# Optimization experiments

Measured on AMD Instinct MI355X. Metric: run time of the kernel, lower is better.

## Reference

```python
import jax, jax.numpy as jnp
import numpy as np
import math

N, E, H, A = 50000, 800000, 128, 8
D = H // A


def setup_inputs() -> dict:
    key = jax.random.key(0)
    ks = jax.random.split(key, 12)
    q = jax.random.normal(ks[0], (N, H), dtype=jnp.float32)
    k = jax.random.normal(ks[1], (N, H), dtype=jnp.float32)
    v = jax.random.normal(ks[2], (N, H), dtype=jnp.float32)
    Wq = jax.random.normal(ks[3], (H, H), dtype=jnp.float32) * 0.05
    bq = jax.random.normal(ks[4], (H,), dtype=jnp.float32) * 0.05
    Wk = jax.random.normal(ks[5], (H, H), dtype=jnp.float32) * 0.05
    bk = jax.random.normal(ks[6], (H,), dtype=jnp.float32) * 0.05
    Wv = jax.random.normal(ks[7], (H, H), dtype=jnp.float32) * 0.05
    bv = jax.random.normal(ks[8], (H,), dtype=jnp.float32) * 0.05
    # Ensure every node id appears at least once in q_indices so that
    # q_indices.unique() == arange(N) and the output shape is static [N, H].
    tail = jax.random.randint(ks[9], (E - N,), 0, N)
    q_indices = jnp.concatenate([jnp.arange(N), tail]).astype(jnp.int32)
    k_indices = jax.random.randint(ks[10], (E,), 0, N).astype(jnp.int32)
    return {"q": q, "k": k, "v": v, "Wq": Wq, "bq": bq, "Wk": Wk, "bk": bk,
            "Wv": Wv, "bv": bv, "q_indices": q_indices, "k_indices": k_indices}


def reference(q, k, v, Wq, bq, Wk, bk, Wv, bv, q_indices, k_indices):
    n = q.shape[0]
    # Gather node features per edge (irregular access).
    qe = q[q_indices]            # [E, H]
    ke = k[k_indices]            # [E, H]
    ve = v[k_indices]            # [E, H]
    # Linear projections (torch Linear: x @ W.T + b), split heads -> [E, A, D].
    Q = (qe @ Wq.T + bq).reshape(-1, A, D)
    K = (ke @ Wk.T + bk).reshape(-1, A, D)
    V = (ve @ Wv.T + bv).reshape(-1, A, D)
    # Per-edge scaled dot-product scores: [E, A].
    scores = jnp.einsum('ead,ead->ea', Q, K) / math.sqrt(D)
    # Segment softmax over edges sharing the same destination node
    # (faithful to the original: plain exp, no max subtraction).
    ex = jnp.exp(scores)                                        # [E, A]
    denom = jax.ops.segment_sum(ex, q_indices, num_segments=n)  # [N, A]
    probs = ex / denom[q_indices]                               # [E, A]
    # Scatter-aggregate weighted values per destination node: [N, A, D].
    ctx = jax.ops.segment_sum(probs[:, :, None] * V, q_indices, num_segments=n)
    # Merge heads -> [N, H].
    return ctx.reshape(n, A * D)
```

## Files before the change

### kernel.cpp

```cpp
#include <hip/hip_runtime.h>
#include <hip/hip_bf16.h>

#define HDIM 128
#define LDS_STRIDE 136

typedef __attribute__((ext_vector_type(8))) short bf16x8;
typedef __attribute__((ext_vector_type(4))) float f32x4;

__device__ inline unsigned short f2bf(float f) {
    return __builtin_bit_cast(unsigned short, __float2bfloat16(f));
}
__device__ inline float bflo(unsigned u) { return __uint_as_float(u << 16); }
__device__ inline float bfhi(unsigned u) { return __uint_as_float(u & 0xffff0000u); }

__global__ void init_kernel(int* __restrict__ deg, int n,
                            const float* __restrict__ Wq, const float* __restrict__ Wk,
                            const float* __restrict__ Wv, unsigned short* __restrict__ Wopt) {
    int i = blockIdx.x * 256 + threadIdx.x;
    if (i < n) deg[i] = 0;
    if (i < 3 * HDIM * HDIM) {
        int j  = i & 7;
        int l  = (i >> 3) & 63;
        int ks = (i >> 9) & 3;
        int nt = (i >> 11) & 7;
        int m  = i >> 14;
        const float* W = (m == 0) ? Wq : (m == 1) ? Wk : Wv;
        int row = nt * 16 + (l & 15);
        int col = ks * 32 + ((l >> 4) << 3) + j;
        Wopt[i] = f2bf(W[row * HDIM + col]);
    }
}

__global__ void proj_deg(const float* __restrict__ qin, const float* __restrict__ kin,
                         const float* __restrict__ vin, const unsigned short* __restrict__ Wopt,
                         const float* __restrict__ bq, const float* __restrict__ bk,
                         const float* __restrict__ bv,
                         unsigned short* __restrict__ Qb, unsigned short* __restrict__ Kb,
                         unsigned short* __restrict__ Vb,
                         const int* __restrict__ qidx, int* __restrict__ deg,
                         int* __restrict__ rank, int E, int n, int nbx)
{
    __shared__ unsigned short tile[64 * LDS_STRIDE];

    if (blockIdx.y == 3) {
        int e = blockIdx.x * 256 + threadIdx.x;
        if (e < E) rank[e] = atomicAdd(&deg[qidx[e]], 1);
        return;
    }
    if (blockIdx.x >= (unsigned)nbx) return;

    const int tid  = threadIdx.x;
    const int lane = tid & 63;
    const int wv   = tid >> 6;
    const int m    = blockIdx.y;
    const long node0 = (long)blockIdx.x * 64;

    const float* x = (m == 0) ? qin : (m == 1) ? kin : vin;
    const float* b = (m == 0) ? bq  : (m == 1) ? bk  : bv;
    unsigned short* O = (m == 0) ? Qb : (m == 1) ? Kb : Vb;
    const unsigned short* Wm = Wopt + (size_t)m * HDIM * HDIM;

    #pragma unroll
    for (int it = 0; it < 8; ++it) {
        int f   = it * 256 + tid;
        int row = f >> 5;
        int c4  = f & 31;
        long node = node0 + row;
        float4 val = make_float4(0.f, 0.f, 0.f, 0.f);
        if (node < n) val = ((const float4*)(x + node * HDIM))[c4];
        ushort4 h;
        h.x = f2bf(val.x); h.y = f2bf(val.y); h.z = f2bf(val.z); h.w = f2bf(val.w);
        *(ushort4*)&tile[row * LDS_STRIDE + c4 * 4] = h;
    }
    __syncthreads();

    const int r15  = lane & 15;
    const int quad = lane >> 4;

    bf16x8 af[4];
    #pragma unroll
    for (int ks = 0; ks < 4; ++ks)
        af[ks] = *(const bf16x8*)&tile[(wv * 16 + r15) * LDS_STRIDE + quad * 8 + ks * 32];

    f32x4 acc[8];
    #pragma unroll
    for (int nt = 0; nt < 8; ++nt) {
        acc[nt] = (f32x4){0.f, 0.f, 0.f, 0.f};
        #pragma unroll
        for (int ks = 0; ks < 4; ++ks) {
            const bf16x8 wfrag =
                *(const bf16x8*)(Wm + ((size_t)((nt * 4 + ks) * 64) + lane) * 8);
            acc[nt] = __builtin_amdgcn_mfma_f32_16x16x32_bf16(af[ks], wfrag, acc[nt], 0, 0, 0);
        }
    }
    __syncthreads();

    #pragma unroll
    for (int nt = 0; nt < 8; ++nt) {
        const int c = nt * 16 + r15;
        const float bias = b[c];
        #pragma unroll
        for (int r = 0; r < 4; ++r)
            tile[(wv * 16 + quad * 4 + r) * LDS_STRIDE + c] = f2bf(acc[nt][r] + bias);
    }
    __syncthreads();

    #pragma unroll
    for (int it = 0; it < 4; ++it) {
        int g   = it * 256 + tid;
        int row = g >> 4;
        int col = (g & 15) * 8;
        long node = node0 + row;
        if (node < n) {
            ushort4 lo = *(const ushort4*)&tile[row * LDS_STRIDE + col];
            ushort4 hi = *(const ushort4*)&tile[row * LDS_STRIDE + col + 4];
            uint4 out4;
            out4.x = (unsigned)lo.x | ((unsigned)lo.y << 16);
            out4.y = (unsigned)lo.z | ((unsigned)lo.w << 16);
            out4.z = (unsigned)hi.x | ((unsigned)hi.y << 16);
            out4.w = (unsigned)hi.z | ((unsigned)hi.w << 16);
            *(uint4*)&O[node * HDIM + col] = out4;
        }
    }
}

__global__ void scan_block(const int* __restrict__ deg, int* __restrict__ offs,
                           int* __restrict__ bsum, int n) {
    __shared__ int ws[17];
    const int tid = threadIdx.x;
    const int lane = tid & 63, wv = tid >> 6;
    int i = blockIdx.x * 1024 + tid;
    int v = (i < n) ? deg[i] : 0;
    int sc = v;
    #pragma unroll
    for (int d = 1; d < 64; d <<= 1) {
        int t = __shfl_up(sc, d, 64);
        if (lane >= d) sc += t;
    }
    if (lane == 63) ws[wv] = sc;
    __syncthreads();
    if (tid == 0) {
        int base = 0;
        #pragma unroll
        for (int w = 0; w < 16; ++w) { int t = ws[w]; ws[w] = base; base += t; }
        ws[16] = base;
    }
    __syncthreads();
    if (i < n) offs[i] = ws[wv] + (sc - v);
    if (tid == 0) bsum[blockIdx.x] = ws[16];
}

__global__ void scan_addtops(const int* __restrict__ bsum, int* __restrict__ offs,
                             int n, int E, int nb) {
    __shared__ int s_base;
    const int tid = threadIdx.x;
    if (tid < 64) {
        int v = (tid < nb) ? bsum[tid] : 0;
        int sc = v;
        #pragma unroll
        for (int d = 1; d < 64; d <<= 1) {
            int t = __shfl_up(sc, d, 64);
            if (tid >= d) sc += t;
        }
        if (tid == blockIdx.x) s_base = sc - v;
    }
    __syncthreads();
    int i = blockIdx.x * 1024 + tid;
    if (i < n) offs[i] += s_base;
    if (blockIdx.x == 0 && tid == 0) offs[n] = E;
}

__global__ void fill_kernel(const int* __restrict__ qidx, const int* __restrict__ kidx,
                            const int* __restrict__ offs, const int* __restrict__ rank,
                            int* __restrict__ srcl, int E) {
    int e = blockIdx.x * blockDim.x + threadIdx.x;
    if (e < E) srcl[offs[qidx[e]] + rank[e]] = kidx[e];
}

__global__ void agg_kernel(const uint2* __restrict__ Q2, const uint2* __restrict__ K2,
                           const uint2* __restrict__ V2,
                           const int* __restrict__ offs, const int* __restrict__ srcl,
                           float* __restrict__ out, int n)
{
    const int tid  = threadIdx.x;
    const int l32  = tid & 31;
    const int node = blockIdx.x * 8 + (tid >> 5);
    if (node >= n) return;

    const uint2 qp = Q2[(size_t)node * 32 + l32];
    const float qx = bflo(qp.x), qy = bfhi(qp.x), qz = bflo(qp.y), qw = bfhi(qp.y);

    float dsum = 0.f, a0 = 0.f, a1 = 0.f, a2 = 0.f, a3 = 0.f;
    const int beg = offs[node], end = offs[node + 1];
    const int srcbase = tid & 32;

#define EDGE_STEP(kp, vp)                                                      \
    {                                                                          \
        float part = qx * bflo((kp).x) + qy * bfhi((kp).x)                     \
                   + qz * bflo((kp).y) + qw * bfhi((kp).y);                    \
        part += __shfl_xor(part, 1, 64);                                       \
        part += __shfl_xor(part, 2, 64);                                       \
        float w = __expf(part * 0.25f);                                        \
        dsum += w;                                                             \
        a0 += w * bflo((vp).x); a1 += w * bfhi((vp).x);                        \
        a2 += w * bflo((vp).y); a3 += w * bfhi((vp).y);                        \
    }

    for (int base = beg; base < end; base += 32) {
        int cnt = min(32, end - base);
        int my = (base + l32 < end) ? srcl[base + l32] : 0;
        int j = 0;
        for (; j + 2 <= cnt; j += 2) {
            int s0 = __shfl(my, srcbase + j,     64);
            int s1 = __shfl(my, srcbase + j + 1, 64);
            uint2 k0 = K2[(size_t)s0 * 32 + l32];
            uint2 v0 = V2[(size_t)s0 * 32 + l32];
            uint2 k1 = K2[(size_t)s1 * 32 + l32];
            uint2 v1 = V2[(size_t)s1 * 32 + l32];
            EDGE_STEP(k0, v0); EDGE_STEP(k1, v1);
        }
        for (; j < cnt; ++j) {
            int s = __shfl(my, srcbase + j, 64);
            uint2 kk = K2[(size_t)s * 32 + l32];
            uint2 vv = V2[(size_t)s * 32 + l32];
            EDGE_STEP(kk, vv);
        }
    }
#undef EDGE_STEP

    float inv = 1.f / dsum;
    float4 r = make_float4(a0 * inv, a1 * inv, a2 * inv, a3 * inv);
    *(float4*)&out[(size_t)node * HDIM + l32 * 4] = r;
}

extern "C" void kernel_launch(void* const* d_in, const int* in_sizes, int n_in,
                              void* d_out, int out_size, void* d_ws, size_t ws_size,
                              hipStream_t stream) {
    const float* q  = (const float*)d_in[0];
    const float* k  = (const float*)d_in[1];
    const float* v  = (const float*)d_in[2];
    const float* Wq = (const float*)d_in[3];
    const float* bq = (const float*)d_in[4];
    const float* Wk = (const float*)d_in[5];
    const float* bk = (const float*)d_in[6];
    const float* Wv = (const float*)d_in[7];
    const float* bv = (const float*)d_in[8];
    const int* qidx = (const int*)d_in[9];
    const int* kidx = (const int*)d_in[10];
    float* out = (float*)d_out;

    const int N = in_sizes[0] / HDIM;
    const int E = in_sizes[9];

    char* p = (char*)d_ws;
    unsigned short* Qb = (unsigned short*)p; p += (size_t)N * HDIM * sizeof(unsigned short);
    unsigned short* Kb = (unsigned short*)p; p += (size_t)N * HDIM * sizeof(unsigned short);
    unsigned short* Vb = (unsigned short*)p; p += (size_t)N * HDIM * sizeof(unsigned short);
    unsigned short* Wopt = (unsigned short*)p; p += (size_t)3 * HDIM * HDIM * sizeof(unsigned short);
    int* deg  = (int*)p; p += (size_t)N * sizeof(int);
    int* offs = (int*)p; p += (size_t)(N + 1) * sizeof(int);
    int* bsum = (int*)p; p += 64 * sizeof(int);
    int* rank = (int*)p; p += (size_t)E * sizeof(int);
    int* srcl = (int*)p; p += (size_t)E * sizeof(int);

    const int nbx = (N + 63) / 64;
    const int neb = (E + 255) / 256;
    const int nb  = (N + 1023) / 1024;
    const int initn = (N > 3 * HDIM * HDIM) ? N : 3 * HDIM * HDIM;

    init_kernel<<<(initn + 255) / 256, 256, 0, stream>>>(deg, N, Wq, Wk, Wv, Wopt);
    {
        dim3 grid((nbx > neb) ? nbx : neb, 4);
        proj_deg<<<grid, 256, 0, stream>>>(q, k, v, Wopt, bq, bk, bv, Qb, Kb, Vb,
                                           qidx, deg, rank, E, N, nbx);
    }
    scan_block<<<nb, 1024, 0, stream>>>(deg, offs, bsum, N);
    scan_addtops<<<nb, 1024, 0, stream>>>(bsum, offs, N, E, nb);
    fill_kernel<<<neb, 256, 0, stream>>>(qidx, kidx, offs, rank, srcl, E);
    agg_kernel<<<(N + 7) / 8, 256, 0, stream>>>((const uint2*)Qb, (const uint2*)Kb,
                                                (const uint2*)Vb, offs, srcl, out, N);
}
```

Baseline: 253.7 us.

## Compact proj/degree grid with interleaved blocks and process four edges per thread

Replaces the 2D grid (where many blocks in the projection rows exited early) with a 1D grid that interleaves degree-counting blocks evenly among projection blocks. Degree counting and the CSR fill now handle four edges per thread using int4 loads. This is meant to cut idle and early-exit blocks, mix atomic-heavy and compute-heavy work on the same CUs, and reduce load instruction count. In exchange it adds per-block index arithmetic and a tail path for edge counts not divisible by four.

After: 233.9 us. 1.08x faster.

```diff
diff --git a/kernel.cpp b/kernel.cpp
--- a/kernel.cpp
+++ b/kernel.cpp
@@ -38,22 +38,40 @@
                          unsigned short* __restrict__ Qb, unsigned short* __restrict__ Kb,
                          unsigned short* __restrict__ Vb,
                          const int* __restrict__ qidx, int* __restrict__ deg,
-                         int* __restrict__ rank, int E, int n, int nbx)
+                         int* __restrict__ rank, int E, int n, int nbx, int ndeg, int ntot)
 {
     __shared__ unsigned short tile[64 * LDS_STRIDE];
 
-    if (blockIdx.y == 3) {
-        int e = blockIdx.x * 256 + threadIdx.x;
-        if (e < E) rank[e] = atomicAdd(&deg[qidx[e]], 1);
+    const int id     = blockIdx.x;
+    const int before = (int)(((long)id * ndeg) / ntot);
+    const bool isdeg = (int)(((long)(id + 1) * ndeg) / ntot) > before;
+
+    if (isdeg) {
+        const int e0 = before * 1024 + (int)threadIdx.x * 4;
+        if (e0 + 4 <= E) {
+            const int4 qi = *(const int4*)&qidx[e0];
+            int4 r;
+            r.x = atomicAdd(&deg[qi.x], 1);
+            r.y = atomicAdd(&deg[qi.y], 1);
+            r.z = atomicAdd(&deg[qi.z], 1);
+            r.w = atomicAdd(&deg[qi.w], 1);
+            *(int4*)&rank[e0] = r;
+        } else {
+            #pragma unroll
+            for (int j = 0; j < 4; ++j)
+                if (e0 + j < E) rank[e0 + j] = atomicAdd(&deg[qidx[e0 + j]], 1);
+        }
         return;
     }
-    if (blockIdx.x >= (unsigned)nbx) return;
+
+    const int pid = id - before;
+    const int m   = pid / nbx;
+    const int bx  = pid - m * nbx;
 
     const int tid  = threadIdx.x;
     const int lane = tid & 63;
     const int wv   = tid >> 6;
-    const int m    = blockIdx.y;
-    const long node0 = (long)blockIdx.x * 64;
+    const long node0 = (long)bx * 64;
 
     const float* x = (m == 0) ? qin : (m == 1) ? kin : vin;
     const float* b = (m == 0) ? bq  : (m == 1) ? bk  : bv;
@@ -173,8 +191,20 @@
 __global__ void fill_kernel(const int* __restrict__ qidx, const int* __restrict__ kidx,
                             const int* __restrict__ offs, const int* __restrict__ rank,
                             int* __restrict__ srcl, int E) {
-    int e = blockIdx.x * blockDim.x + threadIdx.x;
-    if (e < E) srcl[offs[qidx[e]] + rank[e]] = kidx[e];
+    int e0 = (blockIdx.x * 256 + (int)threadIdx.x) * 4;
+    if (e0 + 4 <= E) {
+        const int4 qi = *(const int4*)&qidx[e0];
+        const int4 ki = *(const int4*)&kidx[e0];
+        const int4 rk = *(const int4*)&rank[e0];
+        srcl[offs[qi.x] + rk.x] = ki.x;
+        srcl[offs[qi.y] + rk.y] = ki.y;
+        srcl[offs[qi.z] + rk.z] = ki.z;
+        srcl[offs[qi.w] + rk.w] = ki.w;
+    } else {
+        #pragma unroll
+        for (int j = 0; j < 4; ++j)
+            if (e0 + j < E) srcl[offs[qidx[e0 + j]] + rank[e0 + j]] = kidx[e0 + j];
+    }
 }
 
 __global__ void agg_kernel(const uint2* __restrict__ Q2, const uint2* __restrict__ K2,
@@ -263,20 +293,19 @@
     int* rank = (int*)p; p += (size_t)E * sizeof(int);
     int* srcl = (int*)p; p += (size_t)E * sizeof(int);
 
-    const int nbx = (N + 63) / 64;
-    const int neb = (E + 255) / 256;
-    const int nb  = (N + 1023) / 1024;
+    const int nbx  = (N + 63) / 64;
+    const int ndeg = (E + 1023) / 1024;
+    const int ntot = 3 * nbx + ndeg;
+    const int nfb  = (E + 1023) / 1024;
+    const int nb   = (N + 1023) / 1024;
     const int initn = (N > 3 * HDIM * HDIM) ? N : 3 * HDIM * HDIM;
 
     init_kernel<<<(initn + 255) / 256, 256, 0, stream>>>(deg, N, Wq, Wk, Wv, Wopt);
-    {
-        dim3 grid((nbx > neb) ? nbx : neb, 4);
-        proj_deg<<<grid, 256, 0, stream>>>(q, k, v, Wopt, bq, bk, bv, Qb, Kb, Vb,
-                                           qidx, deg, rank, E, N, nbx);
-    }
+    proj_deg<<<ntot, 256, 0, stream>>>(q, k, v, Wopt, bq, bk, bv, Qb, Kb, Vb,
+                                       qidx, deg, rank, E, N, nbx, ndeg, ntot);
     scan_block<<<nb, 1024, 0, stream>>>(deg, offs, bsum, N);
     scan_addtops<<<nb, 1024, 0, stream>>>(bsum, offs, N, E, nb);
-    fill_kernel<<<neb, 256, 0, stream>>>(qidx, kidx, offs, rank, srcl, E);
+    fill_kernel<<<nfb, 256, 0, stream>>>(qidx, kidx, offs, rank, srcl, E);
     agg_kernel<<<(N + 7) / 8, 256, 0, stream>>>((const uint2*)Qb, (const uint2*)Kb,
                                                 (const uint2*)Vb, offs, srcl, out, N);
 }
```
